# Kernel tuning notes

Hardware: AMD Instinct MI355X
Metric: run time of the kernel (lower is better)

The kernel has to match this reference:

```python
import jax, jax.numpy as jnp
import numpy as np

H, W = 512, 512          # image_size
N = 10000                # num gaussians (point cloud size)
NUM_VIEWS = 4
PATCH = 40               # original uses arange(v-20, v+20) -> 40px window


def setup_inputs() -> dict:
    key = jax.random.key(0)
    ks = jax.random.split(key, 6)
    means = jax.random.normal(ks[0], (N, 3), dtype=jnp.float32) * 0.5
    log_scales = jnp.log(0.1) + 0.1 * jax.random.normal(ks[1], (N, 3), dtype=jnp.float32)
    q = jax.random.normal(ks[2], (N, 4), dtype=jnp.float32)
    quats = q / jnp.linalg.norm(q, axis=1, keepdims=True)
    shs = jax.random.normal(ks[3], (N, 3, 16), dtype=jnp.float32) * 0.1  # (sh_degree+1)^2 = 16
    opacities = jnp.full((N, 1), 0.5, dtype=jnp.float32)
    # Camera poses: small yaw sweep looking at the origin from z=+5 so points project in-frame.
    poses = []
    for a in np.linspace(-0.1, 0.1, NUM_VIEWS):
        Rm = np.array([[np.cos(a), 0.0, np.sin(a)],
                       [0.0, 1.0, 0.0],
                       [-np.sin(a), 0.0, np.cos(a)]], dtype=np.float32)
        P = np.eye(4, dtype=np.float32)
        P[:3, :3] = Rm
        P[:3, 3] = np.array([0.0, 0.0, 5.0], dtype=np.float32)
        poses.append(P)
    poses = jnp.asarray(np.stack(poses))
    intrinsics = jnp.asarray(np.array([[500.0, 0.0, 256.0],
                                       [0.0, 500.0, 256.0],
                                       [0.0, 0.0, 1.0]], dtype=np.float32))
    return {"poses": poses, "intrinsics": intrinsics, "means": means,
            "log_scales": log_scales, "quats": quats, "shs": shs, "opacities": opacities}


def _quat_to_mat(q):
    # q: (N,4) wxyz -> (N,3,3), same formula as the torch module
    w, x, y, z = q[:, 0], q[:, 1], q[:, 2], q[:, 3]
    r0 = jnp.stack([1 - 2 * (y * y + z * z), 2 * (x * y - w * z), 2 * (x * z + w * y)], -1)
    r1 = jnp.stack([2 * (x * y + w * z), 1 - 2 * (x * x + z * z), 2 * (y * z - w * x)], -1)
    r2 = jnp.stack([2 * (x * z - w * y), 2 * (y * z + w * x), 1 - 2 * (x * x + y * y)], -1)
    return jnp.stack([r0, r1, r2], -2)


def _render_view(pose, K, means, log_scales, quats, shs, opacities):
    Rm = pose[:3, :3]
    t = pose[:3, 3]
    p_cam = means @ Rm.T + t                      # (N,3)
    p_proj = p_cam @ K.T                          # (N,3)
    uv = p_proj[:, :2] / (p_proj[:, 2:3] + 1e-8)  # (N,2)
    u = jnp.trunc(uv[:, 0]).astype(jnp.int32)     # int(uv) truncation as in python int()
    v = jnp.trunc(uv[:, 1]).astype(jnp.int32)
    valid = (p_cam[:, 2] >= 0.1) & (u >= 0) & (u < W) & (v >= 0) & (v < H)

    scales = jnp.exp(log_scales)                  # (N,3); module uses scale (not scale^2)
    Rg = _quat_to_mat(quats)                      # (N,3,3)
    cov = jnp.einsum('nij,nj,nkj->nik', Rg, scales, Rg)  # R diag(s) R^T
    a, b = cov[:, 0, 0], cov[:, 0, 1]
    c, d = cov[:, 1, 0], cov[:, 1, 1]
    det = a * d - b * c
    inv = jnp.stack([jnp.stack([d, -b], -1), jnp.stack([-c, a], -1)], -2) / det[:, None, None]  # inverse of cov[:2,:2]

    off = jnp.arange(PATCH, dtype=jnp.int32) - PATCH // 2  # -20..19, matches arange(v-20, v+20)
    yy = jnp.broadcast_to(v[:, None, None] + off[None, :, None], (N, PATCH, PATCH))
    xx = jnp.broadcast_to(u[:, None, None] + off[None, None, :], (N, PATCH, PATCH))
    pos = jnp.stack([xx, yy], -1).astype(jnp.float32) - uv[:, None, None, :]  # (N,40,40,2)
    expo = -0.5 * jnp.einsum('nyxi,nij,nyxj->nyx', pos, inv, pos)
    g = jnp.exp(jnp.clip(expo, -10.0, 0.0))

    inb = (yy >= 0) & (yy < H) & (xx >= 0) & (xx < W)
    mask = valid[:, None, None] & inb & (g > 0.001)

    color = jax.nn.sigmoid(shs[:, :, 0])          # (N,3)
    op = jax.nn.sigmoid(opacities)                # (N,1)
    contrib = jnp.where(mask, g, 0.0)[..., None] * (op * color)[:, None, None, :]  # (N,40,40,3)

    image = jnp.zeros((H, W, 3), jnp.float32)
    image = image.at[jnp.clip(yy, 0, H - 1), jnp.clip(xx, 0, W - 1)].add(contrib)
    return image


def reference(poses, intrinsics, means, log_scales, quats, shs, opacities):
    # loop over a small fixed number of views (matches forward's per-view loop)
    imgs = [_render_view(poses[i], intrinsics, means, log_scales, quats, shs, opacities)
            for i in range(NUM_VIEWS)]
    return jnp.stack(imgs)  # (num_views, H, W, 3)
```

## Files before the change

### kernel.cpp

```cpp
#include <hip/hip_runtime.h>

#define IMG_H 512
#define IMG_W 512
#define NGAUSS 10000
#define N_VIEWS 4
#define PATCH 40

#define QMAX 13.815511f

__device__ __forceinline__ float fast_sigmoid(float x) {
    return 1.0f / (1.0f + __expf(-x));
}

__global__ __launch_bounds__(256) void gs_fused_kernel(
    const float* __restrict__ poses,
    const float* __restrict__ Km,
    const float* __restrict__ means,
    const float* __restrict__ log_scales,
    const float* __restrict__ quats,
    const float* __restrict__ shs,
    const float* __restrict__ opac,
    float* __restrict__ out)
{
    const int n = (blockIdx.x << 3) + (threadIdx.x >> 5);
    if (n >= NGAUSS) return;
    const int lane = threadIdx.x & 31;

    const float m0 = means[n * 3 + 0];
    const float m1 = means[n * 3 + 1];
    const float m2 = means[n * 3 + 2];

    const float qw = quats[n * 4 + 0];
    const float qx = quats[n * 4 + 1];
    const float qy = quats[n * 4 + 2];
    const float qz = quats[n * 4 + 3];
    const float R00 = 1.0f - 2.0f * (qy * qy + qz * qz);
    const float R01 = 2.0f * (qx * qy - qw * qz);
    const float R02 = 2.0f * (qx * qz + qw * qy);
    const float R10 = 2.0f * (qx * qy + qw * qz);
    const float R11 = 1.0f - 2.0f * (qx * qx + qz * qz);
    const float R12 = 2.0f * (qy * qz - qw * qx);

    const float s0 = __expf(log_scales[n * 3 + 0]);
    const float s1 = __expf(log_scales[n * 3 + 1]);
    const float s2 = __expf(log_scales[n * 3 + 2]);

    const float a  = R00 * R00 * s0 + R01 * R01 * s1 + R02 * R02 * s2;
    const float b  = R00 * R10 * s0 + R01 * R11 * s1 + R02 * R12 * s2;
    const float dd = R10 * R10 * s0 + R11 * R11 * s1 + R12 * R12 * s2;

    const float det = a * dd - b * b;
    const float i00 =  dd / det;
    const float i01 = -b  / det;
    const float i11 =  a  / det;

    const float rx = sqrtf(QMAX * a)  + 0.5f;
    const float ry = sqrtf(QMAX * dd) + 0.5f;

    const float op = fast_sigmoid(opac[n]);
    const float w0 = op * fast_sigmoid(shs[n * 48 +  0]);
    const float w1 = op * fast_sigmoid(shs[n * 48 + 16]);
    const float w2 = op * fast_sigmoid(shs[n * 48 + 32]);

    const int rsel = lane >> 4;
    const int sub  = lane & 15;
    const int px   = sub / 3;
    const int ch   = sub - 3 * px;
    const float wch = (ch == 0) ? w0 : ((ch == 1) ? w1 : w2);

    #pragma unroll
    for (int view = 0; view < N_VIEWS; ++view) {
        const float* P = poses + view * 16;

        const float Xc = P[0] * m0 + P[1] * m1 + P[2]  * m2 + P[3];
        const float Yc = P[4] * m0 + P[5] * m1 + P[6]  * m2 + P[7];
        const float Zc = P[8] * m0 + P[9] * m1 + P[10] * m2 + P[11];

        const float ppx = Km[0] * Xc + Km[1] * Yc + Km[2] * Zc;
        const float ppy = Km[3] * Xc + Km[4] * Yc + Km[5] * Zc;
        const float ppz = Km[6] * Xc + Km[7] * Yc + Km[8] * Zc;

        const float denom = ppz + 1e-8f;
        const float uvx = ppx / denom;
        const float uvy = ppy / denom;

        const int u = (int)uvx;
        const int v = (int)uvy;

        if (!((Zc >= 0.1f) && (u >= 0) && (u < IMG_W) && (v >= 0) && (v < IMG_H)))
            continue;

        int xlo = (int)ceilf (uvx - rx);
        int xhi = (int)floorf(uvx + rx);
        int ylo = (int)ceilf (uvy - ry);
        int yhi = (int)floorf(uvy + ry);
        xlo = max(xlo, max(u - PATCH / 2, 0));
        xhi = min(xhi, min(u + PATCH / 2 - 1, IMG_W - 1));
        ylo = max(ylo, max(v - PATCH / 2, 0));
        yhi = min(yhi, min(v + PATCH / 2 - 1, IMG_H - 1));

        const int wx = xhi - xlo + 1;
        const int wy = yhi - ylo + 1;
        if (wx <= 0 || wy <= 0) continue;

        float* img = out + (size_t)view * IMG_H * IMG_W * 3;

        if (wx <= 5 && wy <= 6) {
            const int xx = xlo + px;
            const bool colok = (xx <= xhi);

            const float dx = (float)xx - uvx;
            const float A  = i00 * dx * dx;
            const float B  = 2.0f * i01 * dx;
            const float C  = i11;

            #pragma unroll
            for (int it = 0; it < 3; ++it) {
                const int yy = ylo + (it << 1) + rsel;
                const bool rowok = (yy <= yhi);

                const float dy = (float)yy - uvy;
                const float q  = A + dy * (B + C * dy);
                const float g  = __expf(fminf(fmaxf(-0.5f * q, -10.0f), 0.0f));

                if (colok && rowok && (g > 0.001f)) {
                    atomicAdd(img + ((size_t)yy * IMG_W + xx) * 3 + ch, g * wch);
                }
            }
        } else {
            const int area = wx * wy;
            for (int p = lane; p < area; p += 32) {
                const int iy = p / wx;
                const int ix = p - iy * wx;
                const int yy = ylo + iy;
                const int xx = xlo + ix;

                const float dx = (float)xx - uvx;
                const float dy = (float)yy - uvy;
                const float q  = dx * (i00 * dx + i01 * dy) + dy * (i01 * dx + i11 * dy);
                const float g  = __expf(fminf(fmaxf(-0.5f * q, -10.0f), 0.0f));

                if (g > 0.001f) {
                    float* pp = img + ((size_t)yy * IMG_W + xx) * 3;
                    atomicAdd(pp + 0, g * w0);
                    atomicAdd(pp + 1, g * w1);
                    atomicAdd(pp + 2, g * w2);
                }
            }
        }
    }
}

extern "C" void kernel_launch(void* const* d_in, const int* in_sizes, int n_in,
                              void* d_out, int out_size, void* d_ws, size_t ws_size,
                              hipStream_t stream) {
    const float* poses      = (const float*)d_in[0];
    const float* intrinsics = (const float*)d_in[1];
    const float* means      = (const float*)d_in[2];
    const float* log_scales = (const float*)d_in[3];
    const float* quats      = (const float*)d_in[4];
    const float* shs        = (const float*)d_in[5];
    const float* opac       = (const float*)d_in[6];
    float* out = (float*)d_out;

    const int nblocks = (NGAUSS + 7) / 8;
    gs_fused_kernel<<<nblocks, 256, 0, stream>>>(
        poses, intrinsics, means, log_scales, quats, shs, opac, out);
}
```

Baseline: 75.44 us.

## Replace atomic scatter splatting with tile binning and per-pixel gather rendering

Splits the single scatter kernel into three: zeroing per-tile counters, binning each gaussian-view pair into 16x16 screen tiles with its projected parameters, and a render pass where each block owns one tile and accumulates its listed gaussians in registers. This is meant to remove the heavy float atomicAdd traffic on the output image, replacing it with one plain store per pixel. In exchange it adds two extra launches, integer atomics on the tile counters, and workspace traffic for the lists. Each tile list is capped at a fixed size, so gaussians beyond that cap would be silently dropped. Empty tiles are never written, so the output still relies on being zeroed beforehand.

```diff
diff --git a/kernel.cpp b/kernel.cpp
--- a/kernel.cpp
+++ b/kernel.cpp
@@ -8,11 +8,26 @@
 
 #define QMAX 13.815511f
 
+#define TILE 16
+#define TILES_X (IMG_W / TILE)
+#define TILES_Y (IMG_H / TILE)
+#define NTILES (TILES_X * TILES_Y)
+#define NTILES_ALL (N_VIEWS * NTILES)
+#define CAP 2048
+
+#define WS_PARAMS_OFF (64 * 1024)
+#define WS_LISTS_OFF  (2 * 1024 * 1024)
+
 __device__ __forceinline__ float fast_sigmoid(float x) {
     return 1.0f / (1.0f + __expf(-x));
 }
 
-__global__ __launch_bounds__(256) void gs_fused_kernel(
+__global__ __launch_bounds__(256) void zero_counts(int* __restrict__ counts) {
+    const int i = blockIdx.x * 256 + threadIdx.x;
+    if (i < NTILES_ALL) counts[i] = 0;
+}
+
+__global__ __launch_bounds__(256) void gs_bin(
     const float* __restrict__ poses,
     const float* __restrict__ Km,
     const float* __restrict__ means,
@@ -20,11 +35,14 @@
     const float* __restrict__ quats,
     const float* __restrict__ shs,
     const float* __restrict__ opac,
-    float* __restrict__ out)
+    int*   __restrict__ counts,
+    float* __restrict__ params,
+    int*   __restrict__ lists)
 {
-    const int n = (blockIdx.x << 3) + (threadIdx.x >> 5);
-    if (n >= NGAUSS) return;
-    const int lane = threadIdx.x & 31;
+    const int t = blockIdx.x * 256 + threadIdx.x;
+    if (t >= NGAUSS * N_VIEWS) return;
+    const int view = t / NGAUSS;
+    const int n    = t - view * NGAUSS;
 
     const float m0 = means[n * 3 + 0];
     const float m1 = means[n * 3 + 1];
@@ -62,93 +80,97 @@
     const float w1 = op * fast_sigmoid(shs[n * 48 + 16]);
     const float w2 = op * fast_sigmoid(shs[n * 48 + 32]);
 
-    const int rsel = lane >> 4;
-    const int sub  = lane & 15;
-    const int px   = sub / 3;
-    const int ch   = sub - 3 * px;
-    const float wch = (ch == 0) ? w0 : ((ch == 1) ? w1 : w2);
-
-    #pragma unroll
-    for (int view = 0; view < N_VIEWS; ++view) {
-        const float* P = poses + view * 16;
-
-        const float Xc = P[0] * m0 + P[1] * m1 + P[2]  * m2 + P[3];
-        const float Yc = P[4] * m0 + P[5] * m1 + P[6]  * m2 + P[7];
-        const float Zc = P[8] * m0 + P[9] * m1 + P[10] * m2 + P[11];
-
-        const float ppx = Km[0] * Xc + Km[1] * Yc + Km[2] * Zc;
-        const float ppy = Km[3] * Xc + Km[4] * Yc + Km[5] * Zc;
-        const float ppz = Km[6] * Xc + Km[7] * Yc + Km[8] * Zc;
-
-        const float denom = ppz + 1e-8f;
-        const float uvx = ppx / denom;
-        const float uvy = ppy / denom;
-
-        const int u = (int)uvx;
-        const int v = (int)uvy;
-
-        if (!((Zc >= 0.1f) && (u >= 0) && (u < IMG_W) && (v >= 0) && (v < IMG_H)))
-            continue;
-
-        int xlo = (int)ceilf (uvx - rx);
-        int xhi = (int)floorf(uvx + rx);
-        int ylo = (int)ceilf (uvy - ry);
-        int yhi = (int)floorf(uvy + ry);
-        xlo = max(xlo, max(u - PATCH / 2, 0));
-        xhi = min(xhi, min(u + PATCH / 2 - 1, IMG_W - 1));
-        ylo = max(ylo, max(v - PATCH / 2, 0));
-        yhi = min(yhi, min(v + PATCH / 2 - 1, IMG_H - 1));
-
-        const int wx = xhi - xlo + 1;
-        const int wy = yhi - ylo + 1;
-        if (wx <= 0 || wy <= 0) continue;
-
-        float* img = out + (size_t)view * IMG_H * IMG_W * 3;
-
-        if (wx <= 5 && wy <= 6) {
-            const int xx = xlo + px;
-            const bool colok = (xx <= xhi);
-
-            const float dx = (float)xx - uvx;
-            const float A  = i00 * dx * dx;
-            const float B  = 2.0f * i01 * dx;
-            const float C  = i11;
-
-            #pragma unroll
-            for (int it = 0; it < 3; ++it) {
-                const int yy = ylo + (it << 1) + rsel;
-                const bool rowok = (yy <= yhi);
-
-                const float dy = (float)yy - uvy;
-                const float q  = A + dy * (B + C * dy);
-                const float g  = __expf(fminf(fmaxf(-0.5f * q, -10.0f), 0.0f));
-
-                if (colok && rowok && (g > 0.001f)) {
-                    atomicAdd(img + ((size_t)yy * IMG_W + xx) * 3 + ch, g * wch);
-                }
-            }
-        } else {
-            const int area = wx * wy;
-            for (int p = lane; p < area; p += 32) {
-                const int iy = p / wx;
-                const int ix = p - iy * wx;
-                const int yy = ylo + iy;
-                const int xx = xlo + ix;
-
-                const float dx = (float)xx - uvx;
-                const float dy = (float)yy - uvy;
-                const float q  = dx * (i00 * dx + i01 * dy) + dy * (i01 * dx + i11 * dy);
-                const float g  = __expf(fminf(fmaxf(-0.5f * q, -10.0f), 0.0f));
-
-                if (g > 0.001f) {
-                    float* pp = img + ((size_t)yy * IMG_W + xx) * 3;
-                    atomicAdd(pp + 0, g * w0);
-                    atomicAdd(pp + 1, g * w1);
-                    atomicAdd(pp + 2, g * w2);
-                }
-            }
+    const float* P = poses + view * 16;
+    const float Xc = P[0] * m0 + P[1] * m1 + P[2]  * m2 + P[3];
+    const float Yc = P[4] * m0 + P[5] * m1 + P[6]  * m2 + P[7];
+    const float Zc = P[8] * m0 + P[9] * m1 + P[10] * m2 + P[11];
+
+    const float ppx = Km[0] * Xc + Km[1] * Yc + Km[2] * Zc;
+    const float ppy = Km[3] * Xc + Km[4] * Yc + Km[5] * Zc;
+    const float ppz = Km[6] * Xc + Km[7] * Yc + Km[8] * Zc;
+
+    const float denom = ppz + 1e-8f;
+    const float uvx = ppx / denom;
+    const float uvy = ppy / denom;
+
+    const int u = (int)uvx;
+    const int v = (int)uvy;
+
+    if (!((Zc >= 0.1f) && (u >= 0) && (u < IMG_W) && (v >= 0) && (v < IMG_H)))
+        return;
+
+    int xlo = (int)ceilf (uvx - rx);
+    int xhi = (int)floorf(uvx + rx);
+    int ylo = (int)ceilf (uvy - ry);
+    int yhi = (int)floorf(uvy + ry);
+    xlo = max(xlo, max(u - PATCH / 2, 0));
+    xhi = min(xhi, min(u + PATCH / 2 - 1, IMG_W - 1));
+    ylo = max(ylo, max(v - PATCH / 2, 0));
+    yhi = min(yhi, min(v + PATCH / 2 - 1, IMG_H - 1));
+    if (xhi < xlo || yhi < ylo) return;
+
+    float* rec = params + (size_t)t * 8;
+    rec[0] = uvx; rec[1] = uvy;
+    rec[2] = i00; rec[3] = i01; rec[4] = i11;
+    rec[5] = w0;  rec[6] = w1;  rec[7] = w2;
+
+    const int tx0 = xlo >> 4, tx1 = xhi >> 4;
+    const int ty0 = ylo >> 4, ty1 = yhi >> 4;
+    for (int ty = ty0; ty <= ty1; ++ty) {
+        for (int tx = tx0; tx <= tx1; ++tx) {
+            const int tile = (view << 10) | (ty << 5) | tx;
+            const int idx = atomicAdd(&counts[tile], 1);
+            if (idx < CAP) lists[(size_t)tile * CAP + idx] = t;
         }
     }
+}
+
+__global__ __launch_bounds__(256) void gs_render(
+    const int*   __restrict__ counts,
+    const float* __restrict__ params,
+    const int*   __restrict__ lists,
+    float* __restrict__ out)
+{
+    const int tileId = blockIdx.x;
+    int cnt = counts[tileId];
+    if (cnt <= 0) return;
+    cnt = min(cnt, CAP);
+
+    const int view = tileId >> 10;
+    const int tl   = tileId & (NTILES - 1);
+    const int px   = ((tl & 31) << 4) + (threadIdx.x & 15);
+    const int py   = ((tl >> 5) << 4) + (threadIdx.x >> 4);
+    const float fx = (float)px;
+    const float fy = (float)py;
+
+    const int* __restrict__ lst = lists + (size_t)tileId * CAP;
+
+    float cr = 0.0f, cg = 0.0f, cb = 0.0f;
+    for (int i = 0; i < cnt; ++i) {
+        const int sid = lst[i];
+        const float4* p4 = reinterpret_cast<const float4*>(params + (size_t)sid * 8);
+        const float4 p0 = p4[0];
+        const float4 p1 = p4[1];
+
+        const float dx = fx - p0.x;
+        const float dy = fy - p0.y;
+        const float q  = p0.z * dx * dx + 2.0f * p0.w * dx * dy + p1.x * dy * dy;
+        const float g  = __expf(fminf(fmaxf(-0.5f * q, -10.0f), 0.0f));
+
+        const int u = (int)p0.x;
+        const int v = (int)p0.y;
+        const bool ok = (g > 0.001f)
+                      & (px >= u - PATCH / 2) & (px <= u + PATCH / 2 - 1)
+                      & (py >= v - PATCH / 2) & (py <= v + PATCH / 2 - 1);
+        if (ok) {
+            cr += g * p1.y;
+            cg += g * p1.z;
+            cb += g * p1.w;
+        }
+    }
+
+    float* o = out + (((size_t)view * IMG_H + py) * IMG_W + px) * 3;
+    o[0] = cr; o[1] = cg; o[2] = cb;
 }
 
 extern "C" void kernel_launch(void* const* d_in, const int* in_sizes, int n_in,
@@ -163,7 +185,16 @@
     const float* opac       = (const float*)d_in[6];
     float* out = (float*)d_out;
 
-    const int nblocks = (NGAUSS + 7) / 8;
-    gs_fused_kernel<<<nblocks, 256, 0, stream>>>(
-        poses, intrinsics, means, log_scales, quats, shs, opac, out);
-}
+    int*   counts = (int*)d_ws;
+    float* params = (float*)((char*)d_ws + WS_PARAMS_OFF);
+    int*   lists  = (int*)((char*)d_ws + WS_LISTS_OFF);
+
+    zero_counts<<<(NTILES_ALL + 255) / 256, 256, 0, stream>>>(counts);
+
+    const int nthreads = NGAUSS * N_VIEWS;
+    gs_bin<<<(nthreads + 255) / 256, 256, 0, stream>>>(
+        poses, intrinsics, means, log_scales, quats, shs, opac,
+        counts, params, lists);
+
+    gs_render<<<NTILES_ALL, 256, 0, stream>>>(counts, params, lists, out);
+}
```

New measurement: 181.3 us. +140.4%, slower.

## Rasterize per image row-band in shared memory with per-block gaussian culling

Applied to the files above, without the earlier changes.

Turns the gaussian-parallel scatter into image-band tiles. Each block owns 8 rows of one view, culls all gaussians against its band into a shared queue, accumulates splats with shared-memory atomics, and writes the band to global memory once with coalesced stores. This removes global atomics and likely the need to pre-zero the output. In exchange every block rescans all 10000 gaussians, each thread walks a whole gaussian serially (load imbalance), and the queue is capped at 3072 entries, so overflow would silently drop gaussians.

```diff
diff --git a/kernel.cpp b/kernel.cpp
--- a/kernel.cpp
+++ b/kernel.cpp
@@ -8,11 +8,17 @@
 
 #define QMAX 13.815511f
 
+#define BAND_ROWS 8
+#define NBANDS_IMG (IMG_H / BAND_ROWS)
+#define NBLOCKS (N_VIEWS * NBANDS_IMG)
+#define QCAP 3072
+#define IMG_FLOATS (BAND_ROWS * IMG_W * 3)
+
 __device__ __forceinline__ float fast_sigmoid(float x) {
     return 1.0f / (1.0f + __expf(-x));
 }
 
-__global__ __launch_bounds__(256) void gs_fused_kernel(
+__global__ __launch_bounds__(256) void gs_band_kernel(
     const float* __restrict__ poses,
     const float* __restrict__ Km,
     const float* __restrict__ means,
@@ -22,63 +28,41 @@
     const float* __restrict__ opac,
     float* __restrict__ out)
 {
-    const int n = (blockIdx.x << 3) + (threadIdx.x >> 5);
-    if (n >= NGAUSS) return;
-    const int lane = threadIdx.x & 31;
+    __shared__ float s_img[IMG_FLOATS];
+    __shared__ int   s_queue[QCAP];
+    __shared__ int   s_qn;
 
-    const float m0 = means[n * 3 + 0];
-    const float m1 = means[n * 3 + 1];
-    const float m2 = means[n * 3 + 2];
+    const int view = blockIdx.x >> 6;
+    const int y0   = (blockIdx.x & 63) << 3;
+    const int tid  = threadIdx.x;
 
-    const float qw = quats[n * 4 + 0];
-    const float qx = quats[n * 4 + 1];
-    const float qy = quats[n * 4 + 2];
-    const float qz = quats[n * 4 + 3];
-    const float R00 = 1.0f - 2.0f * (qy * qy + qz * qz);
-    const float R01 = 2.0f * (qx * qy - qw * qz);
-    const float R02 = 2.0f * (qx * qz + qw * qy);
-    const float R10 = 2.0f * (qx * qy + qw * qz);
-    const float R11 = 1.0f - 2.0f * (qx * qx + qz * qz);
-    const float R12 = 2.0f * (qy * qz - qw * qx);
+    float4* img4 = reinterpret_cast<float4*>(s_img);
+    #pragma unroll
+    for (int i = 0; i < IMG_FLOATS / 4 / 256; ++i)
+        img4[i * 256 + tid] = make_float4(0.f, 0.f, 0.f, 0.f);
+    if (tid == 0) s_qn = 0;
+    __syncthreads();
 
-    const float s0 = __expf(log_scales[n * 3 + 0]);
-    const float s1 = __expf(log_scales[n * 3 + 1]);
-    const float s2 = __expf(log_scales[n * 3 + 2]);
+    const float* P = poses + view * 16;
+    const float P0 = P[0], P1 = P[1], P2  = P[2],  P3  = P[3];
+    const float P4 = P[4], P5 = P[5], P6  = P[6],  P7  = P[7];
+    const float P8 = P[8], P9 = P[9], P10 = P[10], P11 = P[11];
+    const float K0 = Km[0], K1 = Km[1], K2 = Km[2];
+    const float K3 = Km[3], K4 = Km[4], K5 = Km[5];
+    const float K6 = Km[6], K7 = Km[7], K8 = Km[8];
 
-    const float a  = R00 * R00 * s0 + R01 * R01 * s1 + R02 * R02 * s2;
-    const float b  = R00 * R10 * s0 + R01 * R11 * s1 + R02 * R12 * s2;
-    const float dd = R10 * R10 * s0 + R11 * R11 * s1 + R12 * R12 * s2;
+    for (int n = tid; n < NGAUSS; n += 256) {
+        const float m0 = means[n * 3 + 0];
+        const float m1 = means[n * 3 + 1];
+        const float m2 = means[n * 3 + 2];
 
-    const float det = a * dd - b * b;
-    const float i00 =  dd / det;
-    const float i01 = -b  / det;
-    const float i11 =  a  / det;
+        const float Xc = P0 * m0 + P1 * m1 + P2  * m2 + P3;
+        const float Yc = P4 * m0 + P5 * m1 + P6  * m2 + P7;
+        const float Zc = P8 * m0 + P9 * m1 + P10 * m2 + P11;
 
-    const float rx = sqrtf(QMAX * a)  + 0.5f;
-    const float ry = sqrtf(QMAX * dd) + 0.5f;
-
-    const float op = fast_sigmoid(opac[n]);
-    const float w0 = op * fast_sigmoid(shs[n * 48 +  0]);
-    const float w1 = op * fast_sigmoid(shs[n * 48 + 16]);
-    const float w2 = op * fast_sigmoid(shs[n * 48 + 32]);
-
-    const int rsel = lane >> 4;
-    const int sub  = lane & 15;
-    const int px   = sub / 3;
-    const int ch   = sub - 3 * px;
-    const float wch = (ch == 0) ? w0 : ((ch == 1) ? w1 : w2);
-
-    #pragma unroll
-    for (int view = 0; view < N_VIEWS; ++view) {
-        const float* P = poses + view * 16;
-
-        const float Xc = P[0] * m0 + P[1] * m1 + P[2]  * m2 + P[3];
-        const float Yc = P[4] * m0 + P[5] * m1 + P[6]  * m2 + P[7];
-        const float Zc = P[8] * m0 + P[9] * m1 + P[10] * m2 + P[11];
-
-        const float ppx = Km[0] * Xc + Km[1] * Yc + Km[2] * Zc;
-        const float ppy = Km[3] * Xc + Km[4] * Yc + Km[5] * Zc;
-        const float ppz = Km[6] * Xc + Km[7] * Yc + Km[8] * Zc;
+        const float ppx = K0 * Xc + K1 * Yc + K2 * Zc;
+        const float ppy = K3 * Xc + K4 * Yc + K5 * Zc;
+        const float ppz = K6 * Xc + K7 * Yc + K8 * Zc;
 
         const float denom = ppz + 1e-8f;
         const float uvx = ppx / denom;
@@ -90,65 +74,111 @@
         if (!((Zc >= 0.1f) && (u >= 0) && (u < IMG_W) && (v >= 0) && (v < IMG_H)))
             continue;
 
-        int xlo = (int)ceilf (uvx - rx);
-        int xhi = (int)floorf(uvx + rx);
-        int ylo = (int)ceilf (uvy - ry);
-        int yhi = (int)floorf(uvy + ry);
-        xlo = max(xlo, max(u - PATCH / 2, 0));
-        xhi = min(xhi, min(u + PATCH / 2 - 1, IMG_W - 1));
-        ylo = max(ylo, max(v - PATCH / 2, 0));
-        yhi = min(yhi, min(v + PATCH / 2 - 1, IMG_H - 1));
+        const float4 qv = *reinterpret_cast<const float4*>(quats + n * 4);
+        const float qw = qv.x, qx = qv.y, qy = qv.z, qz = qv.w;
+        const float R10 = 2.0f * (qx * qy + qw * qz);
+        const float R11 = 1.0f - 2.0f * (qx * qx + qz * qz);
+        const float R12 = 2.0f * (qy * qz - qw * qx);
 
-        const int wx = xhi - xlo + 1;
-        const int wy = yhi - ylo + 1;
-        if (wx <= 0 || wy <= 0) continue;
+        const float s0 = __expf(log_scales[n * 3 + 0]);
+        const float s1 = __expf(log_scales[n * 3 + 1]);
+        const float s2 = __expf(log_scales[n * 3 + 2]);
 
-        float* img = out + (size_t)view * IMG_H * IMG_W * 3;
+        const float dd = R10 * R10 * s0 + R11 * R11 * s1 + R12 * R12 * s2;
+        const float ry = sqrtf(QMAX * dd) + 0.5f;
 
-        if (wx <= 5 && wy <= 6) {
-            const int xx = xlo + px;
-            const bool colok = (xx <= xhi);
+        const int ylo = max((int)ceilf (uvy - ry), max(v - PATCH / 2, 0));
+        const int yhi = min((int)floorf(uvy + ry), min(v + PATCH / 2 - 1, IMG_H - 1));
+        if (ylo > yhi || ylo > y0 + (BAND_ROWS - 1) || yhi < y0)
+            continue;
 
-            const float dx = (float)xx - uvx;
-            const float A  = i00 * dx * dx;
-            const float B  = 2.0f * i01 * dx;
-            const float C  = i11;
+        const int idx = atomicAdd(&s_qn, 1);
+        if (idx < QCAP) s_queue[idx] = n;
+    }
+    __syncthreads();
 
-            #pragma unroll
-            for (int it = 0; it < 3; ++it) {
-                const int yy = ylo + (it << 1) + rsel;
-                const bool rowok = (yy <= yhi);
+    const int qn = min(s_qn, QCAP);
 
-                const float dy = (float)yy - uvy;
-                const float q  = A + dy * (B + C * dy);
+    for (int i = tid; i < qn; i += 256) {
+        const int n = s_queue[i];
+
+        const float m0 = means[n * 3 + 0];
+        const float m1 = means[n * 3 + 1];
+        const float m2 = means[n * 3 + 2];
+
+        const float4 qv = *reinterpret_cast<const float4*>(quats + n * 4);
+        const float qw = qv.x, qx = qv.y, qy = qv.z, qz = qv.w;
+        const float R00 = 1.0f - 2.0f * (qy * qy + qz * qz);
+        const float R01 = 2.0f * (qx * qy - qw * qz);
+        const float R02 = 2.0f * (qx * qz + qw * qy);
+        const float R10 = 2.0f * (qx * qy + qw * qz);
+        const float R11 = 1.0f - 2.0f * (qx * qx + qz * qz);
+        const float R12 = 2.0f * (qy * qz - qw * qx);
+
+        const float s0 = __expf(log_scales[n * 3 + 0]);
+        const float s1 = __expf(log_scales[n * 3 + 1]);
+        const float s2 = __expf(log_scales[n * 3 + 2]);
+
+        const float a  = R00 * R00 * s0 + R01 * R01 * s1 + R02 * R02 * s2;
+        const float b  = R00 * R10 * s0 + R01 * R11 * s1 + R02 * R12 * s2;
+        const float dd = R10 * R10 * s0 + R11 * R11 * s1 + R12 * R12 * s2;
+
+        const float det = a * dd - b * b;
+        const float i00 =  dd / det;
+        const float i01 = -b  / det;
+        const float i11 =  a  / det;
+
+        const float rx = sqrtf(QMAX * a)  + 0.5f;
+        const float ry = sqrtf(QMAX * dd) + 0.5f;
+
+        const float op = fast_sigmoid(opac[n]);
+        const float w0 = op * fast_sigmoid(shs[n * 48 +  0]);
+        const float w1 = op * fast_sigmoid(shs[n * 48 + 16]);
+        const float w2 = op * fast_sigmoid(shs[n * 48 + 32]);
+
+        const float Xc = P0 * m0 + P1 * m1 + P2  * m2 + P3;
+        const float Yc = P4 * m0 + P5 * m1 + P6  * m2 + P7;
+        const float Zc = P8 * m0 + P9 * m1 + P10 * m2 + P11;
+        const float ppx = K0 * Xc + K1 * Yc + K2 * Zc;
+        const float ppy = K3 * Xc + K4 * Yc + K5 * Zc;
+        const float ppz = K6 * Xc + K7 * Yc + K8 * Zc;
+        const float denom = ppz + 1e-8f;
+        const float uvx = ppx / denom;
+        const float uvy = ppy / denom;
+        const int u = (int)uvx;
+        const int v = (int)uvy;
+
+        const int xlo = max((int)ceilf (uvx - rx), max(u - PATCH / 2, 0));
+        const int xhi = min((int)floorf(uvx + rx), min(u + PATCH / 2 - 1, IMG_W - 1));
+        const int ylo = max(max((int)ceilf (uvy - ry), max(v - PATCH / 2, 0)), y0);
+        const int yhi = min(min((int)floorf(uvy + ry),
+                                min(v + PATCH / 2 - 1, IMG_H - 1)),
+                            y0 + (BAND_ROWS - 1));
+
+        for (int yy = ylo; yy <= yhi; ++yy) {
+            const float dy = (float)yy - uvy;
+            const float qy2  = i11 * dy * dy;
+            const float qy1  = 2.0f * i01 * dy;
+            float* row = s_img + (size_t)(yy - y0) * (IMG_W * 3);
+            for (int xx = xlo; xx <= xhi; ++xx) {
+                const float dx = (float)xx - uvx;
+                const float q  = i00 * dx * dx + qy1 * dx + qy2;
                 const float g  = __expf(fminf(fmaxf(-0.5f * q, -10.0f), 0.0f));
-
-                if (colok && rowok && (g > 0.001f)) {
-                    atomicAdd(img + ((size_t)yy * IMG_W + xx) * 3 + ch, g * wch);
-                }
-            }
-        } else {
-            const int area = wx * wy;
-            for (int p = lane; p < area; p += 32) {
-                const int iy = p / wx;
-                const int ix = p - iy * wx;
-                const int yy = ylo + iy;
-                const int xx = xlo + ix;
-
-                const float dx = (float)xx - uvx;
-                const float dy = (float)yy - uvy;
-                const float q  = dx * (i00 * dx + i01 * dy) + dy * (i01 * dx + i11 * dy);
-                const float g  = __expf(fminf(fmaxf(-0.5f * q, -10.0f), 0.0f));
-
                 if (g > 0.001f) {
-                    float* pp = img + ((size_t)yy * IMG_W + xx) * 3;
-                    atomicAdd(pp + 0, g * w0);
-                    atomicAdd(pp + 1, g * w1);
-                    atomicAdd(pp + 2, g * w2);
+                    atomicAdd(row + xx * 3 + 0, g * w0);
+                    atomicAdd(row + xx * 3 + 1, g * w1);
+                    atomicAdd(row + xx * 3 + 2, g * w2);
                 }
             }
         }
     }
+    __syncthreads();
+
+    float4* o4 = reinterpret_cast<float4*>(
+        out + ((size_t)view * IMG_H + y0) * (IMG_W * 3));
+    #pragma unroll
+    for (int i = 0; i < IMG_FLOATS / 4 / 256; ++i)
+        o4[i * 256 + tid] = img4[i * 256 + tid];
 }
 
 extern "C" void kernel_launch(void* const* d_in, const int* in_sizes, int n_in,
@@ -163,7 +193,6 @@
     const float* opac       = (const float*)d_in[6];
     float* out = (float*)d_out;
 
-    const int nblocks = (NGAUSS + 7) / 8;
-    gs_fused_kernel<<<nblocks, 256, 0, stream>>>(
+    gs_band_kernel<<<NBLOCKS, 256, 0, stream>>>(
         poses, intrinsics, means, log_scales, quats, shs, opac, out);
 }
```

Result: slower. 117.5 us (+55.7%).
